# Optimization experiments

Measured on AMD Instinct MI355X. Metric: run time of the kernel, lower is better.

Reference implementation:

```python
import jax, jax.numpy as jnp
import numpy as np

SC = 11  # window stride / block size; unfold kernel = 3*SC = 33, padding = SC


def _unfold3(x, sc):
    """Equivalent of nn.Unfold(kernel=3*sc, stride=sc, padding=sc) on [b,c,H,W]
    where H, W are multiples of sc. Returns [b, c, 9*sc*sc, n_windows].
    Patch ordering within K differs from torch by a fixed permutation, which is
    immaterial: all contractions over K (mask, softmax, value aggregation) are
    permutation-invariant as long as the same unfold is used everywhere."""
    b, c, H, W = x.shape
    h_sc, w_sc = H // sc, W // sc
    xp = jnp.pad(x, ((0, 0), (0, 0), (sc, sc), (sc, sc)))
    blk = xp.reshape(b, c, h_sc + 2, sc, w_sc + 2, sc)
    # 3x3 neighborhood of sc-blocks around each window
    pat = jnp.stack([blk[:, :, di:di + h_sc, :, dj:dj + w_sc, :]
                     for di in range(3) for dj in range(3)], axis=2)
    # [b,c,9,h_sc,r,w_sc,s] -> [b,c,9,r,s,h_sc,w_sc] -> [b,c,9*sc*sc,n]
    pat = pat.transpose(0, 1, 2, 4, 6, 3, 5)
    return pat.reshape(b, c, 9 * sc * sc, h_sc * w_sc)


def _block_q(x, sc):
    """view(b,c,h_sc,sc,w_sc,sc).permute(0,1,2,4,3,5) -> [b,c,n,sc*sc]"""
    b, c, H, W = x.shape
    h_sc, w_sc = H // sc, W // sc
    y = x.reshape(b, c, h_sc, sc, w_sc, sc).transpose(0, 1, 2, 4, 3, 5)
    return y.reshape(b, c, h_sc * w_sc, sc * sc)


def setup_inputs() -> dict:
    key = jax.random.key(0)
    k1, k2, k3, k4, k5, k6 = jax.random.split(key, 6)
    b, c, h, w = 2, 64, 256, 256
    s = 1.0 / np.sqrt(c)
    return {
        "x_key": jax.random.normal(k1, (b, c, h, w), jnp.float32),
        "x_ref": jax.random.normal(k2, (b, c, h, w), jnp.float32),
        "Wq": jax.random.normal(k3, (c, c), jnp.float32) * s,
        "Wk": jax.random.normal(k4, (c, c), jnp.float32) * s,
        "Wv": jax.random.normal(k5, (c, c), jnp.float32) * s,
        "gamma": jax.random.normal(k6, (1,), jnp.float32) * 0.1,
    }


def reference(x_key, x_ref, Wq, Wk, Wv, gamma):
    sc = SC
    b, c, h_in, w_in = x_key.shape
    x_pad = sc - w_in % sc
    y_pad = sc - h_in % sc
    pad = ((0, 0), (0, 0), (0, y_pad), (0, x_pad))
    fk = jnp.pad(x_key, pad)
    fr = jnp.pad(x_ref, pad)
    b, c, h, w = fk.shape
    h_sc, w_sc = h // sc, w // sc

    # validity mask -> additive attention bias (out-of-image keys penalized)
    fm = jnp.pad(jnp.ones((1, 1, h_in, w_in), fk.dtype), pad)
    fm_k = _unfold3(fm, sc)          # [1,1,K,n]
    fm_q = _block_q(fm, sc)          # [1,1,n,s]
    am = (jnp.einsum('bckn,bcns->bkns', fm_k, fm_q) - 1.0) * 99.0  # [1,K,n,s]

    scale = c ** (-0.5)
    q = jnp.einsum('oi,bihw->bohw', Wq, fk)
    k = jnp.einsum('oi,bihw->bohw', Wk, fr)
    v = jnp.einsum('oi,bihw->bohw', Wv, fr)

    k_u = _unfold3(k, sc) * scale    # [b,c,K,n]
    q_b = _block_q(q, sc)            # [b,c,n,s]
    attn = jnp.einsum('bckn,bcns->bkns', k_u, q_b) + am  # [b,K,n,s]
    attn = jax.nn.softmax(attn, axis=1)

    v_u = _unfold3(v, sc)            # [b,c,K,n]
    r = jnp.einsum('bkns,bckn->bcns', attn, v_u)  # [b,c,n,s]
    r = r.reshape(b, c, h_sc, w_sc, sc, sc).transpose(0, 1, 2, 4, 3, 5)
    r = r.reshape(b, c, h, w)[:, :, :h_in, :w_in]
    return x_ref + r * gamma[0]
```

## Files before the change

### kernel.cpp

```cpp
#include <hip/hip_runtime.h>


typedef unsigned short ushort_t;
typedef unsigned int   uint32;
typedef unsigned long long uint64;
typedef __attribute__((ext_vector_type(8))) short short8;
typedef __attribute__((ext_vector_type(4))) float f32x4;

#define MFMA16(a,b,c) __builtin_amdgcn_mfma_f32_16x16x32_bf16(a,b,c,0,0,0)

#if __has_builtin(__builtin_amdgcn_exp2f)
#define EXP2(x) __builtin_amdgcn_exp2f(x)
#else
#define EXP2(x) exp2f(x)
#endif
#if __has_builtin(__builtin_amdgcn_rcpf)
#define RCP(x) __builtin_amdgcn_rcpf(x)
#else
#define RCP(x) (1.0f/(x))
#endif

#define QPKT_OFF   0u
#define KPKT_OFF   18874368u
#define VPKT_OFF   37748736u

__device__ __forceinline__ ushort_t f2bf(float f){
  union { __bf16 h; ushort_t u; } c;
  c.h = (__bf16)f;
  return c.u;
}

__device__ __forceinline__ uint32 pkbf(float a, float b){
  union { __bf16 h[2]; uint32 u; } c;
  c.h[0] = (__bf16)a;
  c.h[1] = (__bf16)b;
  return c.u;
}

__device__ __forceinline__ void storeK8(ushort_t* __restrict__ base, int nt, int t,
                                        int l15, int h, f32x4 a){
  uint32 lo = pkbf(a[0], a[1]);
  uint32 hi = pkbf(a[2], a[3]);
  int lanep = l15 + 16*((2*t + (h>>1)) & 3);
  size_t off = (size_t)((nt*2 + (t>>1))*64 + lanep)*16 + 8*(h&1);
  *(uint2*)((char*)base + off) = make_uint2(lo, hi);
}

__device__ __forceinline__ short8 ldWfrag(const float* __restrict__ W, int t, int ks,
                                          int l15, int h, float scale){
  const float* p = W + (16*t + l15)*64 + 32*ks + 8*h;
  float4 a = *(const float4*)p;
  float4 b = *(const float4*)(p + 4);
  union { uint4 u; short8 s; } x;
  x.u.x = pkbf(a.x*scale, a.y*scale);
  x.u.y = pkbf(a.z*scale, a.w*scale);
  x.u.z = pkbf(b.x*scale, b.y*scale);
  x.u.w = pkbf(b.z*scale, b.w*scale);
  return x.s;
}

__global__ __launch_bounds__(256) void proj_kernel(
    const float* __restrict__ xk, const float* __restrict__ xr,
    const float* __restrict__ Wq, const float* __restrict__ Wk, const float* __restrict__ Wv,
    ushort_t* __restrict__ qpkt, ushort_t* __restrict__ kpkt, ushort_t* __restrict__ vpkt)
{
  __shared__ __align__(16) float sX[64*192];
  const int tid = threadIdx.x;
  const int lane = tid & 63, wv = tid >> 6;
  const int l15 = lane & 15, h = lane >> 4;
  const int bid = blockIdx.x;
  const bool isQ = bid >= 1152;
  const int id = isQ ? bid - 1152 : bid;
  const int b = id / 576, rem = id % 576, ty = rem / 24, tx = rem % 24;
  const float* xs = (isQ ? xk : xr) + (size_t)b*64*65536;
  const int oy = ty*11, ox = tx*11;
  const int ox3 = ox & 3, xa = ox - ox3;

  #pragma unroll
  for (int i = tid; i < 1024; i += 256) sX[(i>>4)*192 + 176 + (i&15)] = 0.f;

  {
    const int ch = tid >> 2, seg = tid & 3;
    const float* rowp = xs + (size_t)ch*65536 + (size_t)oy*256 + (xa + 4*seg);
    float* sdst = sX + ch*192 + 4*seg;
    if (ty < 23 && tx < 23){
      #pragma unroll
      for (int y = 0; y < 11; ++y)
        *(float4*)(sdst + y*16) = *(const float4*)(rowp + y*256);
    } else {
      const int xg = xa + 4*seg;
      #pragma unroll
      for (int y = 0; y < 11; ++y){
        const bool rk = (oy + y) < 256;
        float4 v;
        v.x = (rk && xg+0 < 256) ? rowp[y*256+0] : 0.f;
        v.y = (rk && xg+1 < 256) ? rowp[y*256+1] : 0.f;
        v.z = (rk && xg+2 < 256) ? rowp[y*256+2] : 0.f;
        v.w = (rk && xg+3 < 256) ? rowp[y*256+3] : 0.f;
        *(float4*)(sdst + y*16) = v;
      }
    }
  }
  __syncthreads();

  const f32x4 zero = {0.f, 0.f, 0.f, 0.f};
  #define XFL(nt, ks, dst) { \
    const int px_ = 16*(nt) + l15; \
    const int y_ = (px_*745) >> 13; \
    const float* pp_ = sX + (32*(ks) + 8*h)*192 + y_*16 + (px_ - y_*11) + ox3; \
    union { uint4 u; short8 s; } r_; \
    r_.u.x = pkbf(pp_[0],    pp_[192]); \
    r_.u.y = pkbf(pp_[384],  pp_[576]); \
    r_.u.z = pkbf(pp_[768],  pp_[960]); \
    r_.u.w = pkbf(pp_[1152], pp_[1344]); \
    dst = r_.s; }

  if (!isQ){
    short8 wkf[4][2], wvf[4][2];
    #pragma unroll
    for (int t = 0; t < 4; ++t){
      wkf[t][0] = ldWfrag(Wk, t, 0, l15, h, 1.f);  wkf[t][1] = ldWfrag(Wk, t, 1, l15, h, 1.f);
      wvf[t][0] = ldWfrag(Wv, t, 0, l15, h, 1.f);  wvf[t][1] = ldWfrag(Wv, t, 1, l15, h, 1.f);
    }
    ushort_t* kb = kpkt + (size_t)id*8192;
    ushort_t* vb = vpkt + (size_t)id*8192;
    const int nt0 = 2*wv, nt1 = 2*wv + 1;
    short8 xf0[2], xf1[2];
    XFL(nt0, 0, xf0[0]); XFL(nt0, 1, xf0[1]);
    XFL(nt1, 0, xf1[0]); XFL(nt1, 1, xf1[1]);
    #pragma unroll
    for (int t = 0; t < 4; ++t){
      f32x4 ak0 = MFMA16(wkf[t][0], xf0[0], zero); ak0 = MFMA16(wkf[t][1], xf0[1], ak0);
      f32x4 ak1 = MFMA16(wkf[t][0], xf1[0], zero); ak1 = MFMA16(wkf[t][1], xf1[1], ak1);
      f32x4 av0 = MFMA16(xf0[0], wvf[t][0], zero); av0 = MFMA16(xf0[1], wvf[t][1], av0);
      f32x4 av1 = MFMA16(xf1[0], wvf[t][0], zero); av1 = MFMA16(xf1[1], wvf[t][1], av1);
      storeK8(kb, nt0, t, l15, h, ak0);
      storeK8(kb, nt1, t, l15, h, ak1);
      uint4 pv;
      pv.x = pkbf(av0[0], av0[1]); pv.y = pkbf(av0[2], av0[3]);
      pv.z = pkbf(av1[0], av1[1]); pv.w = pkbf(av1[2], av1[3]);
      *(uint4*)((char*)vb + (size_t)((wv*4 + t)*64 + lane)*16) = pv;
    }
  } else {
    const float C1 = 0.18033688011112042f;
    short8 wqf[4][2];
    #pragma unroll
    for (int t = 0; t < 4; ++t){
      wqf[t][0] = ldWfrag(Wq, t, 0, l15, h, C1);  wqf[t][1] = ldWfrag(Wq, t, 1, l15, h, C1);
    }
    ushort_t* qb = qpkt + (size_t)id*8192;
    #pragma unroll
    for (int nn = 0; nn < 2; ++nn){
      const int nt = 2*wv + nn;
      short8 xf[2];
      XFL(nt, 0, xf[0]); XFL(nt, 1, xf[1]);
      #pragma unroll
      for (int t = 0; t < 4; ++t){
        f32x4 aq = MFMA16(wqf[t][0], xf[0], zero); aq = MFMA16(wqf[t][1], xf[1], aq);
        storeK8(qb, nt, t, l15, h, aq);
      }
    }
  }
  #undef XFL
}

__global__ __launch_bounds__(256) void attn_kernel(
    ushort_t* qpkt,
    const ushort_t* __restrict__ kpkt, const ushort_t* __restrict__ vpkt,
    const float* __restrict__ gamma)
{
  __shared__ __align__(16) char smem[24576];
  const int tid = threadIdx.x;
  const int lane = tid & 63, wave = tid >> 6;
  const int qh = wave & 1, kh = wave >> 1;
  const int win = (blockIdx.x & 7)*144 + (blockIdx.x >> 3);
  const int b = win / 576, wid = win % 576, wy = wid / 24, wx = wid % 24;
  const int l15 = lane & 15, h = lane >> 4;

  short8 qf[4][2];
  {
    const ushort_t* qblk = qpkt + (size_t)win*8192;
    #pragma unroll
    for (int mt = 0; mt < 4; ++mt){
      qf[mt][0] = *(const short8*)(qblk + (size_t)(((4*qh+mt)*2 + 0)*64 + lane)*8);
      qf[mt][1] = *(const short8*)(qblk + (size_t)(((4*qh+mt)*2 + 1)*64 + lane)*8);
    }
  }

  uint64 cks = 0; int nv = 0;
  #pragma unroll
  for (int ck = 0; ck < 9; ++ck){
    const int ty = wy - 1 + ck/3, tx = wx - 1 + ck%3;
    if ((unsigned)ty < 24u && (unsigned)tx < 24u){
      cks |= ((uint64)ck) << (4*nv); ++nv;
    }
  }
  const int nu = 2*nv;

  const f32x4 zz = {0.f,0.f,0.f,0.f};
  f32x4 o[4][4], lsumC[4];
  #pragma unroll
  for (int mt = 0; mt < 4; ++mt){
    lsumC[mt] = zz;
    #pragma unroll
    for (int u = 0; u < 4; ++u) o[mt][u] = zz;
  }
  f32x4 init_i;
  #pragma unroll
  for (int r = 0; r < 4; ++r) init_i[r] = (4*h + r >= 9) ? -1.0e4f : 0.f;
  short8 ones;
  #pragma unroll
  for (int j = 0; j < 8; ++j) ones[j] = (short)0x3F80;

  const int lane16 = lane*16;

  #define ISSUE(KD, VD, u_) { \
    const int t_ = (u_) >> 1, hf_ = (u_) & 1; \
    const int ck_ = (int)((cks >> (4*t_)) & 15); \
    const int cy_ = (ck_*11) >> 5; \
    const size_t tb_ = ((size_t)(b*576 + (wy-1+cy_)*24 + (wx-1+(ck_-3*cy_))) << 14) \
                       + ((size_t)hf_ << 13) + ((size_t)kh << 12) + (size_t)lane16; \
    const char* kg_ = (const char*)kpkt + tb_; \
    const char* vg_ = (const char*)vpkt + tb_; \
    _Pragma("unroll") \
    for (int r_ = 0; r_ < 4; ++r_){ \
      KD[r_] = *(const short8*)(kg_ + r_*1024); \
      VD[r_] = *(const short8*)(vg_ + r_*1024); \
    } }

  #define COMPUTE(KC, VC, u_) { \
    const int t_ = (u_) >> 1, hf_ = (u_) & 1; \
    const int ckv = (int)((cks >> (4*t_)) & 15); \
    const int cyv = (ckv*11) >> 5; \
    const int tyv = wy - 1 + cyv, txv = wx - 1 + (ckv - 3*cyv); \
    const bool ey = (tyv == 23), ex = (txv == 23); \
    const int ntp = 2*hf_ + kh; \
    f32x4 b0, b1; \
    if (ey | ex){ \
      _Pragma("unroll") \
      for (int kt = 0; kt < 2; ++kt){ \
        f32x4 bb; \
        _Pragma("unroll") \
        for (int r = 0; r < 4; ++r){ \
          const int kl = 32*ntp + 16*kt + 4*h + r; \
          const int ky = (kl*745) >> 13, kx = kl - ky*11; \
          bool ok = (kl < 121) && (!ey || ky < 3) && (!ex || kx < 3); \
          bb[r] = ok ? 0.f : -1.0e4f; \
        } \
        if (kt) b1 = bb; else b0 = bb; \
      } \
    } else { \
      b0 = zz; \
      b1 = (hf_ & kh) ? init_i : zz;    \
    } \
    __builtin_amdgcn_s_setprio(1); \
    _Pragma("unroll") \
    for (int mt = 0; mt < 4; ++mt){ \
      f32x4 s0 = MFMA16(KC[0], qf[mt][0], b0); s0 = MFMA16(KC[1], qf[mt][1], s0); \
      f32x4 s1 = MFMA16(KC[2], qf[mt][0], b1); s1 = MFMA16(KC[3], qf[mt][1], s1); \
      float p[8]; \
      _Pragma("unroll") \
      for (int r = 0; r < 4; ++r){ \
        p[r]   = EXP2(s0[r]); \
        p[4+r] = EXP2(s1[r]); \
      } \
      union { uint4 uu; short8 s; } af; \
      af.uu.x = pkbf(p[0], p[1]); af.uu.y = pkbf(p[2], p[3]); \
      af.uu.z = pkbf(p[4], p[5]); af.uu.w = pkbf(p[6], p[7]); \
      o[mt][0] = MFMA16(af.s, VC[0], o[mt][0]); \
      o[mt][1] = MFMA16(af.s, VC[1], o[mt][1]); \
      o[mt][2] = MFMA16(af.s, VC[2], o[mt][2]); \
      o[mt][3] = MFMA16(af.s, VC[3], o[mt][3]); \
      lsumC[mt] = MFMA16(af.s, ones, lsumC[mt]); \
    } \
    __builtin_amdgcn_s_setprio(0); }

  short8 kA[4], vA[4], kB[4], vB[4], kC[4], vC[4];

  ISSUE(kA, vA, 0);
  ISSUE(kB, vB, 1);
  ISSUE(kC, vC, 2);

  {
    int u = 0;
    #pragma unroll 1
    while (true){
      COMPUTE(kA, vA, u); if (u + 3 < nu) ISSUE(kA, vA, u + 3);
      if (++u >= nu) break;
      COMPUTE(kB, vB, u); if (u + 3 < nu) ISSUE(kB, vB, u + 3);
      if (++u >= nu) break;
      COMPUTE(kC, vC, u); if (u + 3 < nu) ISSUE(kC, vC, u + 3);
      if (++u >= nu) break;
    }
  }
  #undef ISSUE
  #undef COMPUTE

  __syncthreads();
  {
    float* base = (float*)(smem + qh*12288);
    if (kh){
      #pragma unroll
      for (int mt = 0; mt < 4; ++mt){
        *(f32x4*)(base + (mt*2+0)*256 + lane*4) = o[mt][0];
        *(f32x4*)(base + (mt*2+1)*256 + lane*4) = o[mt][1];
        *(f32x4*)(base + (8+mt)*256 + lane*4)   = lsumC[mt];
      }
    }
  }
  __syncthreads();
  if (!kh){
    float* base = (float*)(smem + qh*12288);
    #pragma unroll
    for (int mt = 0; mt < 4; ++mt){
      o[mt][0] += *(const f32x4*)(base + (mt*2+0)*256 + lane*4);
      o[mt][1] += *(const f32x4*)(base + (mt*2+1)*256 + lane*4);
      lsumC[mt] += *(const f32x4*)(base + (8+mt)*256 + lane*4);
    }
  }
  __syncthreads();
  {
    float* base2 = (float*)(smem + qh*8192);
    if (kh){
      #pragma unroll
      for (int mt = 0; mt < 4; ++mt){
        *(f32x4*)(base2 + (mt*2+0)*256 + lane*4) = o[mt][2];
        *(f32x4*)(base2 + (mt*2+1)*256 + lane*4) = o[mt][3];
      }
    }
  }
  __syncthreads();
  if (!kh){
    float* base2 = (float*)(smem + qh*8192);
    #pragma unroll
    for (int mt = 0; mt < 4; ++mt){
      o[mt][2] += *(const f32x4*)(base2 + (mt*2+0)*256 + lane*4);
      o[mt][3] += *(const f32x4*)(base2 + (mt*2+1)*256 + lane*4);
    }
    const float gm = gamma[0];
    ushort_t* rb = qpkt + (size_t)win*8192 + (size_t)qh*4096;
    #pragma unroll
    for (int mt = 0; mt < 4; ++mt){
      #pragma unroll
      for (int r = 0; r < 4; ++r){
        const float wg = gm * RCP(lsumC[mt][r]);
        const int qs = 16*mt + 4*h + r;
        #pragma unroll
        for (int u = 0; u < 4; ++u)
          rb[(size_t)qs*64 + 16*u + l15] = f2bf(wg * o[mt][u][r]);
      }
    }
  }
}

__global__ __launch_bounds__(256) void ep_kernel(
    const float* __restrict__ xref, const ushort_t* __restrict__ rbuf,
    float* __restrict__ out)
{
  __shared__ float tile[64][65];
  const int tid = threadIdx.x;
  const int bidx = blockIdx.x;
  const int xc = bidx & 3, y = (bidx >> 2) & 255, b = bidx >> 10;
  const int wy = (y*745) >> 13, qy = y - wy*11;
  {
    const int ch = tid & 63, xs4 = tid >> 6;
    #pragma unroll
    for (int xi = 0; xi < 16; ++xi){
      const int xl = xi*4 + xs4;
      const int x = xc*64 + xl;
      const int wx = (x*745) >> 13, qx = x - wx*11;
      const size_t ridx = (size_t)(b*576 + wy*24 + wx)*8192 + (size_t)(qy*11 + qx)*64 + ch;
      tile[xl][ch] = __uint_as_float(((uint32)rbuf[ridx]) << 16);
    }
  }
  __syncthreads();
  {
    const int xl = tid & 63, cg = tid >> 6;
    const size_t base = (size_t)b*4194304 + (size_t)y*256 + xc*64 + xl;
    #pragma unroll
    for (int ci = 0; ci < 16; ++ci){
      const int c2 = ci*4 + cg;
      const size_t idx = base + (size_t)c2*65536;
      out[idx] = xref[idx] + tile[xl][c2];
    }
  }
}

extern "C" void kernel_launch(void* const* d_in, const int* in_sizes, int n_in,
                              void* d_out, int out_size, void* d_ws, size_t ws_size,
                              hipStream_t stream)
{
  const float* xk = (const float*)d_in[0];
  const float* xr = (const float*)d_in[1];
  const float* Wq = (const float*)d_in[2];
  const float* Wk = (const float*)d_in[3];
  const float* Wv = (const float*)d_in[4];
  const float* gm = (const float*)d_in[5];
  float* out = (float*)d_out;
  char* ws = (char*)d_ws;
  ushort_t* qp = (ushort_t*)(ws + QPKT_OFF);
  ushort_t* kp = (ushort_t*)(ws + KPKT_OFF);
  ushort_t* vp = (ushort_t*)(ws + VPKT_OFF);
  (void)in_sizes; (void)n_in; (void)out_size; (void)ws_size;

  proj_kernel<<<2304, 256, 0, stream>>>(xk, xr, Wq, Wk, Wv, qp, kp, vp);
  attn_kernel<<<1152, 256, 0, stream>>>(qp, kp, vp, gm);
  ep_kernel<<<2048, 256, 0, stream>>>(xr, qp, out);
}
```

Measured before the change: 251.6 us.

## Split attention work by query quarters per wave, removing cross-wave LDS reduction

Each wave now owns 32 query rows and iterates over every key quarter-tile itself, instead of pairing waves that split keys and then reduce partial outputs through shared memory. This removes the LDS buffer, four __syncthreads and the reduction code, and halves per-wave accumulator and Q-fragment registers. The prefetch depth drops from three to two stages and launch bounds ask for three blocks per CU to raise occupancy. In exchange each wave loads every K/V tile, so K/V global traffic per block doubles, and the shallower prefetch may expose more latency.

```diff
diff --git a/kernel.cpp b/kernel.cpp
--- a/kernel.cpp
+++ b/kernel.cpp
@@ -164,26 +164,24 @@
   #undef XFL
 }
 
-__global__ __launch_bounds__(256) void attn_kernel(
+__global__ __launch_bounds__(256, 3) void attn_kernel(
     ushort_t* qpkt,
     const ushort_t* __restrict__ kpkt, const ushort_t* __restrict__ vpkt,
     const float* __restrict__ gamma)
 {
-  __shared__ __align__(16) char smem[24576];
   const int tid = threadIdx.x;
-  const int lane = tid & 63, wave = tid >> 6;
-  const int qh = wave & 1, kh = wave >> 1;
+  const int lane = tid & 63, qq = tid >> 6;
   const int win = (blockIdx.x & 7)*144 + (blockIdx.x >> 3);
   const int b = win / 576, wid = win % 576, wy = wid / 24, wx = wid % 24;
   const int l15 = lane & 15, h = lane >> 4;
 
-  short8 qf[4][2];
+  short8 qf[2][2];
   {
     const ushort_t* qblk = qpkt + (size_t)win*8192;
     #pragma unroll
-    for (int mt = 0; mt < 4; ++mt){
-      qf[mt][0] = *(const short8*)(qblk + (size_t)(((4*qh+mt)*2 + 0)*64 + lane)*8);
-      qf[mt][1] = *(const short8*)(qblk + (size_t)(((4*qh+mt)*2 + 1)*64 + lane)*8);
+    for (int mt = 0; mt < 2; ++mt){
+      qf[mt][0] = *(const short8*)(qblk + (size_t)(((2*qq+mt)*2 + 0)*64 + lane)*8);
+      qf[mt][1] = *(const short8*)(qblk + (size_t)(((2*qq+mt)*2 + 1)*64 + lane)*8);
     }
   }
 
@@ -195,12 +193,12 @@
       cks |= ((uint64)ck) << (4*nv); ++nv;
     }
   }
-  const int nu = 2*nv;
+  const int nu = 4*nv;
 
   const f32x4 zz = {0.f,0.f,0.f,0.f};
-  f32x4 o[4][4], lsumC[4];
-  #pragma unroll
-  for (int mt = 0; mt < 4; ++mt){
+  f32x4 o[2][4], lsumC[2];
+  #pragma unroll
+  for (int mt = 0; mt < 2; ++mt){
     lsumC[mt] = zz;
     #pragma unroll
     for (int u = 0; u < 4; ++u) o[mt][u] = zz;
@@ -215,11 +213,11 @@
   const int lane16 = lane*16;
 
   #define ISSUE(KD, VD, u_) { \
-    const int t_ = (u_) >> 1, hf_ = (u_) & 1; \
+    const int t_ = (u_) >> 2, qtr_ = (u_) & 3; \
     const int ck_ = (int)((cks >> (4*t_)) & 15); \
     const int cy_ = (ck_*11) >> 5; \
     const size_t tb_ = ((size_t)(b*576 + (wy-1+cy_)*24 + (wx-1+(ck_-3*cy_))) << 14) \
-                       + ((size_t)hf_ << 13) + ((size_t)kh << 12) + (size_t)lane16; \
+                       + ((size_t)qtr_ << 12) + (size_t)lane16; \
     const char* kg_ = (const char*)kpkt + tb_; \
     const char* vg_ = (const char*)vpkt + tb_; \
     _Pragma("unroll") \
@@ -229,12 +227,11 @@
     } }
 
   #define COMPUTE(KC, VC, u_) { \
-    const int t_ = (u_) >> 1, hf_ = (u_) & 1; \
+    const int t_ = (u_) >> 2, qtr_ = (u_) & 3; \
     const int ckv = (int)((cks >> (4*t_)) & 15); \
     const int cyv = (ckv*11) >> 5; \
     const int tyv = wy - 1 + cyv, txv = wx - 1 + (ckv - 3*cyv); \
     const bool ey = (tyv == 23), ex = (txv == 23); \
-    const int ntp = 2*hf_ + kh; \
     f32x4 b0, b1; \
     if (ey | ex){ \
       _Pragma("unroll") \
@@ -242,7 +239,7 @@
         f32x4 bb; \
         _Pragma("unroll") \
         for (int r = 0; r < 4; ++r){ \
-          const int kl = 32*ntp + 16*kt + 4*h + r; \
+          const int kl = 32*qtr_ + 16*kt + 4*h + r; \
           const int ky = (kl*745) >> 13, kx = kl - ky*11; \
           bool ok = (kl < 121) && (!ey || ky < 3) && (!ex || kx < 3); \
           bb[r] = ok ? 0.f : -1.0e4f; \
@@ -251,11 +248,11 @@
       } \
     } else { \
       b0 = zz; \
-      b1 = (hf_ & kh) ? init_i : zz;    \
+      b1 = (qtr_ == 3) ? init_i : zz;    \
     } \
     __builtin_amdgcn_s_setprio(1); \
     _Pragma("unroll") \
-    for (int mt = 0; mt < 4; ++mt){ \
+    for (int mt = 0; mt < 2; ++mt){ \
       f32x4 s0 = MFMA16(KC[0], qf[mt][0], b0); s0 = MFMA16(KC[1], qf[mt][1], s0); \
       f32x4 s1 = MFMA16(KC[2], qf[mt][0], b1); s1 = MFMA16(KC[3], qf[mt][1], s1); \
       float p[8]; \
@@ -275,80 +272,35 @@
     } \
     __builtin_amdgcn_s_setprio(0); }
 
-  short8 kA[4], vA[4], kB[4], vB[4], kC[4], vC[4];
+  short8 kA[4], vA[4], kB[4], vB[4];
 
   ISSUE(kA, vA, 0);
   ISSUE(kB, vB, 1);
-  ISSUE(kC, vC, 2);
 
   {
     int u = 0;
     #pragma unroll 1
     while (true){
-      COMPUTE(kA, vA, u); if (u + 3 < nu) ISSUE(kA, vA, u + 3);
+      COMPUTE(kA, vA, u); if (u + 2 < nu) ISSUE(kA, vA, u + 2);
       if (++u >= nu) break;
-      COMPUTE(kB, vB, u); if (u + 3 < nu) ISSUE(kB, vB, u + 3);
-      if (++u >= nu) break;
-      COMPUTE(kC, vC, u); if (u + 3 < nu) ISSUE(kC, vC, u + 3);
+      COMPUTE(kB, vB, u); if (u + 2 < nu) ISSUE(kB, vB, u + 2);
       if (++u >= nu) break;
     }
   }
   #undef ISSUE
   #undef COMPUTE
 
-  __syncthreads();
-  {
-    float* base = (float*)(smem + qh*12288);
-    if (kh){
+  const float gm = gamma[0];
+  ushort_t* rb = qpkt + (size_t)win*8192;
+  #pragma unroll
+  for (int mt = 0; mt < 2; ++mt){
+    #pragma unroll
+    for (int r = 0; r < 4; ++r){
+      const float wg = gm * RCP(lsumC[mt][r]);
+      const int qs = 32*qq + 16*mt + 4*h + r;
       #pragma unroll
-      for (int mt = 0; mt < 4; ++mt){
-        *(f32x4*)(base + (mt*2+0)*256 + lane*4) = o[mt][0];
-        *(f32x4*)(base + (mt*2+1)*256 + lane*4) = o[mt][1];
-        *(f32x4*)(base + (8+mt)*256 + lane*4)   = lsumC[mt];
-      }
-    }
-  }
-  __syncthreads();
-  if (!kh){
-    float* base = (float*)(smem + qh*12288);
-    #pragma unroll
-    for (int mt = 0; mt < 4; ++mt){
-      o[mt][0] += *(const f32x4*)(base + (mt*2+0)*256 + lane*4);
-      o[mt][1] += *(const f32x4*)(base + (mt*2+1)*256 + lane*4);
-      lsumC[mt] += *(const f32x4*)(base + (8+mt)*256 + lane*4);
-    }
-  }
-  __syncthreads();
-  {
-    float* base2 = (float*)(smem + qh*8192);
-    if (kh){
-      #pragma unroll
-      for (int mt = 0; mt < 4; ++mt){
-        *(f32x4*)(base2 + (mt*2+0)*256 + lane*4) = o[mt][2];
-        *(f32x4*)(base2 + (mt*2+1)*256 + lane*4) = o[mt][3];
-      }
-    }
-  }
-  __syncthreads();
-  if (!kh){
-    float* base2 = (float*)(smem + qh*8192);
-    #pragma unroll
-    for (int mt = 0; mt < 4; ++mt){
-      o[mt][2] += *(const f32x4*)(base2 + (mt*2+0)*256 + lane*4);
-      o[mt][3] += *(const f32x4*)(base2 + (mt*2+1)*256 + lane*4);
-    }
-    const float gm = gamma[0];
-    ushort_t* rb = qpkt + (size_t)win*8192 + (size_t)qh*4096;
-    #pragma unroll
-    for (int mt = 0; mt < 4; ++mt){
-      #pragma unroll
-      for (int r = 0; r < 4; ++r){
-        const float wg = gm * RCP(lsumC[mt][r]);
-        const int qs = 16*mt + 4*h + r;
-        #pragma unroll
-        for (int u = 0; u < 4; ++u)
-          rb[(size_t)qs*64 + 16*u + l15] = f2bf(wg * o[mt][u][r]);
-      }
+      for (int u = 0; u < 4; ++u)
+        rb[(size_t)qs*64 + 16*u + l15] = f2bf(wg * o[mt][u][r]);
     }
   }
 }
```

New measurement: 295.8 us. +17.6%, slower.
